# Optimization experiments

Measured on AMD Instinct MI355X. Metric: run time of the kernel, lower is better.

The kernel has to match this reference:

```python
import jax, jax.numpy as jnp
import numpy as np
from jax import lax

# ---- Loihi neuron constants (params['neuron'], params['simulation']) ----
VTH_MANT = 80
THETA = VTH_MANT * (1 << 6)          # 5120, vThMant scaled by 2^6 weight resolution
I_DECAY = 1024                        # current decay (12-bit fixed point)
V_DECAY = 128                         # voltage decay (12-bit fixed point)
WGT_EXP = 0
WGT_SCALE = 1 << (6 + WGT_EXP)        # 64
TS = 1.0

def _loihi_srm_kernel():
    # integer Loihi simulation of the PSP impulse response (slayerLoihi._calculateLoihiPSP)
    u = 1 << (6 + WGT_EXP)
    v = u
    ker = [v]
    while ker[-1] > 0:
        u = (u * (4096 - I_DECAY)) >> 12
        v = ((v * (4096 - V_DECAY)) >> 12) + u
        ker.append(v)
    return np.asarray(ker, np.float32) / (1 << 6)

SRM_KERNEL = _loihi_srm_kernel()      # ~180 taps, ker[0] = 1

def psp(x):
    # causal FIR over time: y[t] = sum_k x[t-k] * ker[k];  x: [B, C, T]
    B, C, T = x.shape
    K = SRM_KERNEL.shape[0]
    w = jnp.asarray(SRM_KERNEL[::-1].copy()).reshape(1, 1, K).astype(x.dtype)
    y = lax.conv_general_dilated(x.reshape(B * C, 1, T), w, (1,), [(K - 1, 0)],
                                 dimension_numbers=('NCH', 'OIH', 'NCH'))
    return y.reshape(B, C, T)

def _decay(x, d):
    # sign-symmetric arithmetic-shift decay, exactly as the Loihi CUDA kernel
    s = jnp.where(x >= 0, 1, -1).astype(jnp.int32)
    return s * ((s * x * (4096 - d)) >> 12)

def spike_loihi(w):
    # quantized integrate-and-fire; w: [B, C, T] float weighted input
    x = jnp.trunc(w * (WGT_SCALE / TS)).astype(jnp.int32)   # C-style int() truncation
    xt = jnp.moveaxis(x, -1, 0)                             # [T, B, C]
    z = jnp.zeros(x.shape[:-1], jnp.int32)
    def step(carry, xi):
        u, v = carry
        un = _decay(u, I_DECAY) + xi
        vn = _decay(v, V_DECAY) + un
        sp = vn >= THETA
        vn = jnp.where(sp, 0, vn)                           # hard reset on spike
        return (un, vn), (sp, vn)
    _, (s, vrec) = lax.scan(step, (z, z), xt)
    spike = jnp.moveaxis(s, 0, -1).astype(w.dtype) / TS
    voltage = jnp.moveaxis(vrec, 0, -1).astype(w.dtype)
    return spike, voltage

def delay_shift(x):
    # delayShift(x, 1): one-tick axonal delay along time
    return jnp.concatenate([jnp.zeros_like(x[..., :1]), x[..., :-1]], axis=-1)

def setup_inputs():
    key = jax.random.key(0)
    k1, k2, k3 = jax.random.split(key, 3)
    B, CIN, HID, COUT, T = 32, 512, 1024, 256, 512
    spike_input = (jax.random.uniform(k1, (B, CIN, 1, 1, T)) < 0.05).astype(jnp.float32)
    W1 = jax.random.normal(k2, (HID, CIN), jnp.float32) * 0.2
    W2 = jax.random.normal(k3, (COUT, HID), jnp.float32) * 0.2
    return {"spike_input": spike_input, "W1": W1, "W2": W2}

def reference(spike_input, W1, W2):
    x = spike_input[:, :, 0, 0, :]                          # [B, Cin, T]
    s1, _ = spike_loihi(psp(jnp.einsum('oi,bit->bot', W1, x)))
    s1 = delay_shift(s1)
    s2, _ = spike_loihi(psp(jnp.einsum('oh,bht->bot', W2, s1)))
    s2 = delay_shift(s2)
    return s2[:, :, None, None, :]                          # [B, Cout, 1, 1, T]
```

## Files before the change

### kernel.cpp

```cpp
#include <hip/hip_runtime.h>


#pragma clang fp contract(off)

constexpr int kT     = 512;
constexpr int kCIN   = 512;
constexpr int kHID   = 1024;
constexpr int kCOUT  = 256;
constexpr int kB     = 32;
constexpr int kTHETA = 5120;
constexpr int kOT1   = 16;
constexpr int kOT2   = 8;
constexpr int kHBP1  = 20;
constexpr int kHBP2  = 12;
constexpr int kSBP   = 516;
constexpr int kCURP  = 520;

__device__ __forceinline__ float2 pkmul(const float2 a, const float b) {
    return make_float2(a.x * b, a.y * b);
}
__device__ __forceinline__ float2 pkadd(const float2 a, const float2 b) {
    return make_float2(a.x + b.x, a.y + b.y);
}

__device__ __forceinline__ int decay_i(int x, int mult) {
    unsigned ax = (x >= 0) ? (unsigned)x : (0u - (unsigned)x);
    unsigned p  = ax * (unsigned)mult;
    int sh = ((int)p) >> 12;
    return (x >= 0) ? sh : (int)(0u - (unsigned)sh);
}

__device__ __forceinline__ void build_ker_f(float* kerf) {
    int u = 64, v = 64;
    kerf[0] = 1.0f;
    int i = 1;
    while (v > 0 && i < 96) {
        u = (u * 3072) >> 12;
        v = ((v * 3968) >> 12) + u;
        kerf[i++] = (float)v * 0.015625f;
    }
}

__global__ __launch_bounds__(256) void k0_pack(const float* __restrict__ X,
                                               unsigned* __restrict__ XPW) {
    const int tid = blockIdx.x * 256 + threadIdx.x;
    const int b = tid >> 13, rem = tid & 8191, w = rem >> 9, t = rem & 511;
    const float* xp = X + ((size_t)(b * kCIN + w * 32)) * kT + t;
    unsigned m = 0;
#pragma unroll
    for (int k = 0; k < 32; ++k)
        m |= (xp[(size_t)k * kT] != 0.0f ? 1u : 0u) << k;
    XPW[tid] = m;
}

#define GW16(MW, BASE) { unsigned m_ = (MW); while (m_) { \
    const int bi_ = __ffs(m_) - 1; m_ &= m_ - 1; const int ii_ = (BASE) + bi_; \
    const float4 f0 = *reinterpret_cast<const float4*>(&w0[ii_ * 4]); \
    const float4 f1 = *reinterpret_cast<const float4*>(&w1[ii_ * 4]); \
    const float4 f2 = *reinterpret_cast<const float4*>(&w2[ii_ * 4]); \
    const float4 f3 = *reinterpret_cast<const float4*>(&w3[ii_ * 4]); \
    A0 = pkadd(A0, make_float2(f0.x, f0.y)); A1 = pkadd(A1, make_float2(f0.z, f0.w)); \
    A2 = pkadd(A2, make_float2(f1.x, f1.y)); A3 = pkadd(A3, make_float2(f1.z, f1.w)); \
    A4 = pkadd(A4, make_float2(f2.x, f2.y)); A5 = pkadd(A5, make_float2(f2.z, f2.w)); \
    A6 = pkadd(A6, make_float2(f3.x, f3.y)); A7 = pkadd(A7, make_float2(f3.z, f3.w)); } }

__global__ __launch_bounds__(512) void k1_fused(const unsigned* __restrict__ XPW,
                                                const float* __restrict__ W,
                                                unsigned char* __restrict__ SPT) {
    __shared__ __align__(16) unsigned char regn[40960];
    __shared__ unsigned char sbuf[kOT1 * kSBP];
    __shared__ float kerf[96];

    float* w0  = reinterpret_cast<float*>(regn);
    float* w1  = reinterpret_cast<float*>(regn + 8192);
    float* w2  = reinterpret_cast<float*>(regn + 16384);
    float* w3  = reinterpret_cast<float*>(regn + 24576);
    float* hbf = reinterpret_cast<float*>(regn);
    int*   cur = reinterpret_cast<int*>(regn);

    const int t     = threadIdx.x;
    const int b     = blockIdx.x >> 6;
    const int oblk  = blockIdx.x & 63;
    const int obase = oblk * kOT1;

    if (t == 0) build_ker_f(kerf);
    for (int idx = t; idx < kOT1 * kCIN; idx += 512) {
        const int j = idx >> 9, i = idx & 511;
        float* wq = reinterpret_cast<float*>(regn + (j >> 2) * 8192);
        wq[i * 4 + (j & 3)] = W[(size_t)(obase + j) * kCIN + i];
    }
    __syncthreads();

    const unsigned* xw = XPW + ((size_t)b * 16) * kT + t;
    float2 A0 = make_float2(0.f, 0.f), A1 = A0, A2 = A0, A3 = A0,
           A4 = A0, A5 = A0, A6 = A0, A7 = A0;
    {
        const unsigned m0=xw[0],    m1=xw[512],  m2=xw[1024], m3=xw[1536],
                       m4=xw[2048], m5=xw[2560], m6=xw[3072], m7=xw[3584],
                       m8=xw[4096], m9=xw[4608], mA=xw[5120], mB=xw[5632],
                       mC=xw[6144], mD=xw[6656], mE=xw[7168], mF=xw[7680];
        GW16(m0,0)   GW16(m1,32)  GW16(m2,64)  GW16(m3,96)
        GW16(m4,128) GW16(m5,160) GW16(m6,192) GW16(m7,224)
        GW16(m8,256) GW16(m9,288) GW16(mA,320) GW16(mB,352)
        GW16(mC,384) GW16(mD,416) GW16(mE,448) GW16(mF,480)
    }
    __syncthreads();

    {
        float* hr = hbf + (size_t)t * kHBP1;
        *reinterpret_cast<float4*>(hr + 0)  = make_float4(A0.x, A0.y, A1.x, A1.y);
        *reinterpret_cast<float4*>(hr + 4)  = make_float4(A2.x, A2.y, A3.x, A3.y);
        *reinterpret_cast<float4*>(hr + 8)  = make_float4(A4.x, A4.y, A5.x, A5.y);
        *reinterpret_cast<float4*>(hr + 12) = make_float4(A6.x, A6.y, A7.x, A7.y);
    }
    __syncthreads();

    float2 c0 = make_float2(0.f, 0.f), c1 = c0, c2 = c0, c3 = c0,
           c4 = c0, c5 = c0, c6 = c0, c7 = c0;
    {
        const int kmax = min(t + 1, 88);
        for (int tau = kmax - 1; tau >= 0; --tau) {
            const float kv = kerf[tau];
            const float* hr = hbf + (size_t)(t - tau) * kHBP1;
            const float4 q0 = *reinterpret_cast<const float4*>(hr + 0);
            const float4 q1 = *reinterpret_cast<const float4*>(hr + 4);
            const float4 q2 = *reinterpret_cast<const float4*>(hr + 8);
            const float4 q3 = *reinterpret_cast<const float4*>(hr + 12);
            c0 = pkadd(c0, pkmul(make_float2(q0.x, q0.y), kv));
            c1 = pkadd(c1, pkmul(make_float2(q0.z, q0.w), kv));
            c2 = pkadd(c2, pkmul(make_float2(q1.x, q1.y), kv));
            c3 = pkadd(c3, pkmul(make_float2(q1.z, q1.w), kv));
            c4 = pkadd(c4, pkmul(make_float2(q2.x, q2.y), kv));
            c5 = pkadd(c5, pkmul(make_float2(q2.z, q2.w), kv));
            c6 = pkadd(c6, pkmul(make_float2(q3.x, q3.y), kv));
            c7 = pkadd(c7, pkmul(make_float2(q3.z, q3.w), kv));
        }
    }
    __syncthreads();

    cur[ 0 * kCURP + t] = (int)(c0.x * 64.0f);
    cur[ 1 * kCURP + t] = (int)(c0.y * 64.0f);
    cur[ 2 * kCURP + t] = (int)(c1.x * 64.0f);
    cur[ 3 * kCURP + t] = (int)(c1.y * 64.0f);
    cur[ 4 * kCURP + t] = (int)(c2.x * 64.0f);
    cur[ 5 * kCURP + t] = (int)(c2.y * 64.0f);
    cur[ 6 * kCURP + t] = (int)(c3.x * 64.0f);
    cur[ 7 * kCURP + t] = (int)(c3.y * 64.0f);
    cur[ 8 * kCURP + t] = (int)(c4.x * 64.0f);
    cur[ 9 * kCURP + t] = (int)(c4.y * 64.0f);
    cur[10 * kCURP + t] = (int)(c5.x * 64.0f);
    cur[11 * kCURP + t] = (int)(c5.y * 64.0f);
    cur[12 * kCURP + t] = (int)(c6.x * 64.0f);
    cur[13 * kCURP + t] = (int)(c6.y * 64.0f);
    cur[14 * kCURP + t] = (int)(c7.x * 64.0f);
    cur[15 * kCURP + t] = (int)(c7.y * 64.0f);
    __syncthreads();

    if (t < kOT1) {
        const int* cr = cur + t * kCURP;
        int u = 0, v = 0;
        sbuf[t * kSBP + 0] = 0;
        for (int s = 0; s < kT; ++s) {
            const int un = (int)((unsigned)decay_i(u, 3072) + (unsigned)cr[s]);
            int vn = (int)((unsigned)decay_i(v, 3968) + (unsigned)un);
            const int sp_ = (vn >= kTHETA) ? 1 : 0;
            if (sp_) vn = 0;
            u = un; v = vn;
            if (s + 1 < kT) sbuf[t * kSBP + s + 1] = (unsigned char)sp_;
        }
    }
    __syncthreads();

#pragma unroll
    for (int h = 0; h < 2; ++h) {
        unsigned byte = 0;
#pragma unroll
        for (int j = 0; j < 8; ++j)
            byte |= (unsigned)sbuf[(h * 8 + j) * kSBP + t] << j;
        SPT[((size_t)b * 128 + oblk * 2 + h) * kT + t] = (unsigned char)byte;
    }
}

#define GW8(MW, BASE) { unsigned m_ = (MW); while (m_) { \
    const int bi_ = __ffs(m_) - 1; m_ &= m_ - 1; const int ii_ = (BASE) + bi_; \
    const float4 lo = *reinterpret_cast<const float4*>(&wlo[ii_ * 4]); \
    const float4 hi = *reinterpret_cast<const float4*>(&whi[ii_ * 4]); \
    A0 = pkadd(A0, make_float2(lo.x, lo.y)); A1 = pkadd(A1, make_float2(lo.z, lo.w)); \
    A2 = pkadd(A2, make_float2(hi.x, hi.y)); A3 = pkadd(A3, make_float2(hi.z, hi.w)); } }

__global__ __launch_bounds__(512) void k2_fused(const unsigned char* __restrict__ SPT,
                                                const float* __restrict__ W,
                                                float* __restrict__ O) {
    __shared__ __align__(16) unsigned char regn[32768];
    __shared__ unsigned char sbuf[kOT2 * kSBP];
    __shared__ float kerf[96];

    float* wlo = reinterpret_cast<float*>(regn);
    float* whi = reinterpret_cast<float*>(regn + 16384);
    float* hbf = reinterpret_cast<float*>(regn);
    int*   cur = reinterpret_cast<int*>(regn);

    const int t     = threadIdx.x;
    const int b     = blockIdx.x >> 5;
    const int obase = (blockIdx.x & 31) * kOT2;

    if (t == 0) build_ker_f(kerf);
    for (int idx = t; idx < kOT2 * kHID; idx += 512) {
        const int j = idx >> 10, i = idx & 1023;
        const float w = W[(size_t)(obase + j) * kHID + i];
        if (j < 4) wlo[i * 4 + j] = w; else whi[i * 4 + (j - 4)] = w;
    }
    __syncthreads();

    const unsigned char* sp = SPT + (size_t)b * (128 * kT) + t;
    float2 A0 = make_float2(0.f, 0.f), A1 = A0, A2 = A0, A3 = A0;
    for (int wd = 0; wd < 32; ++wd) {
        const unsigned b0 = sp[(size_t)(4 * wd + 0) * kT];
        const unsigned b1 = sp[(size_t)(4 * wd + 1) * kT];
        const unsigned b2 = sp[(size_t)(4 * wd + 2) * kT];
        const unsigned b3 = sp[(size_t)(4 * wd + 3) * kT];
        const unsigned m = b0 | (b1 << 8) | (b2 << 16) | (b3 << 24);
        GW8(m, wd * 32)
    }
    __syncthreads();

    {
        float* hr = hbf + (size_t)t * kHBP2;
        *reinterpret_cast<float4*>(hr + 0) = make_float4(A0.x, A0.y, A1.x, A1.y);
        *reinterpret_cast<float4*>(hr + 4) = make_float4(A2.x, A2.y, A3.x, A3.y);
    }
    __syncthreads();

    float2 c0 = make_float2(0.f, 0.f), c1 = c0, c2 = c0, c3 = c0;
    {
        const int kmax = min(t + 1, 88);
        for (int tau = kmax - 1; tau >= 0; --tau) {
            const float kv = kerf[tau];
            const float* hr = hbf + (size_t)(t - tau) * kHBP2;
            const float4 q0 = *reinterpret_cast<const float4*>(hr + 0);
            const float4 q1 = *reinterpret_cast<const float4*>(hr + 4);
            c0 = pkadd(c0, pkmul(make_float2(q0.x, q0.y), kv));
            c1 = pkadd(c1, pkmul(make_float2(q0.z, q0.w), kv));
            c2 = pkadd(c2, pkmul(make_float2(q1.x, q1.y), kv));
            c3 = pkadd(c3, pkmul(make_float2(q1.z, q1.w), kv));
        }
    }
    __syncthreads();

    cur[0 * kCURP + t] = (int)(c0.x * 64.0f);
    cur[1 * kCURP + t] = (int)(c0.y * 64.0f);
    cur[2 * kCURP + t] = (int)(c1.x * 64.0f);
    cur[3 * kCURP + t] = (int)(c1.y * 64.0f);
    cur[4 * kCURP + t] = (int)(c2.x * 64.0f);
    cur[5 * kCURP + t] = (int)(c2.y * 64.0f);
    cur[6 * kCURP + t] = (int)(c3.x * 64.0f);
    cur[7 * kCURP + t] = (int)(c3.y * 64.0f);
    __syncthreads();

    if (t < kOT2) {
        const int* cr = cur + t * kCURP;
        int u = 0, v = 0;
        sbuf[t * kSBP + 0] = 0;
        for (int s = 0; s < kT; ++s) {
            const int un = (int)((unsigned)decay_i(u, 3072) + (unsigned)cr[s]);
            int vn = (int)((unsigned)decay_i(v, 3968) + (unsigned)un);
            const int sp2 = (vn >= kTHETA) ? 1 : 0;
            if (sp2) vn = 0;
            u = un; v = vn;
            if (s + 1 < kT) sbuf[t * kSBP + s + 1] = (unsigned char)sp2;
        }
    }
    __syncthreads();

    for (int idx = t; idx < kOT2 * kT; idx += 512) {
        const int j = idx >> 9, tt = idx & 511;
        O[((size_t)(b * kCOUT + obase + j)) * kT + tt] = (float)sbuf[j * kSBP + tt];
    }
}

__global__ void k_mark(float* __restrict__ out0, float v) {
    if (threadIdx.x == 0 && blockIdx.x == 0) out0[0] = v;
}

extern "C" void kernel_launch(void* const* d_in, const int* in_sizes, int n_in,
                              void* d_out, int out_size, void* d_ws, size_t ws_size,
                              hipStream_t stream) {
    const float* X  = (const float*)d_in[0];
    const float* W1 = (const float*)d_in[1];
    const float* W2 = (const float*)d_in[2];
    float* OUT = (float*)d_out;

    const size_t xpw_bytes = (size_t)kB * 16 * kT * 4;
    const size_t spt_bytes = (size_t)kB * 128 * kT;
    const size_t need = xpw_bytes + spt_bytes;

    if (n_in != 3 || in_sizes[0] != kB * kCIN * kT || in_sizes[1] != kHID * kCIN ||
        in_sizes[2] != kCOUT * kHID || out_size != kB * kCOUT * kT) {
        hipLaunchKernelGGL(k_mark, dim3(1), dim3(64), 0, stream, OUT, 7000001.0f);
        return;
    }
    if (ws_size < need || d_ws == nullptr) {
        const float v = (float)(8000000u + (unsigned)((ws_size >> 10) % 900000));
        hipLaunchKernelGGL(k_mark, dim3(1), dim3(64), 0, stream, OUT, v);
        return;
    }

    unsigned*      xpw = (unsigned*)d_ws;
    unsigned char* spt = (unsigned char*)d_ws + xpw_bytes;

    hipLaunchKernelGGL(k0_pack, dim3(kB * 16 * kT / 256), dim3(256), 0, stream,
                       X, xpw);
    hipLaunchKernelGGL(k1_fused, dim3(kB * (kHID / kOT1)), dim3(512), 0, stream,
                       xpw, W1, spt);
    hipLaunchKernelGGL(k2_fused, dim3(kB * (kCOUT / kOT2)), dim3(512), 0, stream,
                       spt, W2, OUT);
}
```

Baseline: 454.9 us.

## Register-block PSP convolution over time pairs and pack layer-1 spikes as 32-bit words

The causal PSP FIR is restructured so each of 256 threads computes two adjacent timesteps, with hidden rows split into even/odd shared buffers. Each loaded row pair is reused for two outputs, which halves LDS traffic per output. The SRM kernel moves to compile-time constant memory, removing the per-block serial build. The layer-1 spike bitmask is stored as interleaved 16-bit halves, so layer 2 reads one 32-bit word per 32 channels instead of assembling four bytes, and occupancy hints are added to the launch bounds. The trade-off is that only half the threads do the convolution, and the summation order changes, so the float rounding of the accumulations may differ slightly.

Result: faster. 395.9 us (-13.0%).

```diff
diff --git a/kernel.cpp b/kernel.cpp
--- a/kernel.cpp
+++ b/kernel.cpp
@@ -11,10 +11,25 @@
 constexpr int kTHETA = 5120;
 constexpr int kOT1   = 16;
 constexpr int kOT2   = 8;
-constexpr int kHBP1  = 20;
-constexpr int kHBP2  = 12;
+constexpr int kHP1   = 20;
+constexpr int kHP2   = 12;
 constexpr int kSBP   = 516;
-constexpr int kCURP  = 520;
+constexpr int kCURP  = 521;
+
+struct Ker { float v[96]; int n; };
+constexpr Ker mk_ker() {
+    Ker K{}; int u = 64, v = 64; K.v[0] = 1.0f; int i = 1;
+    while (v > 0 && i < 96) {
+        u = (u * 3072) >> 12;
+        v = ((v * 3968) >> 12) + u;
+        K.v[i++] = (float)v / 64.0f;
+    }
+    K.n = i; return K;
+}
+constexpr Ker KER = mk_ker();
+static_assert(KER.n == 88, "SRM kernel length must be 88");
+static_assert(KER.v[87] == 0.0f, "tap 87 must be the exact zero tail tap");
+__device__ __constant__ Ker KERC = mk_ker();
 
 __device__ __forceinline__ float2 pkmul(const float2 a, const float b) {
     return make_float2(a.x * b, a.y * b);
@@ -28,17 +43,6 @@
     unsigned p  = ax * (unsigned)mult;
     int sh = ((int)p) >> 12;
     return (x >= 0) ? sh : (int)(0u - (unsigned)sh);
-}
-
-__device__ __forceinline__ void build_ker_f(float* kerf) {
-    int u = 64, v = 64;
-    kerf[0] = 1.0f;
-    int i = 1;
-    while (v > 0 && i < 96) {
-        u = (u * 3072) >> 12;
-        v = ((v * 3968) >> 12) + u;
-        kerf[i++] = (float)v * 0.015625f;
-    }
 }
 
 __global__ __launch_bounds__(256) void k0_pack(const float* __restrict__ X,
@@ -64,26 +68,35 @@
     A4 = pkadd(A4, make_float2(f2.x, f2.y)); A5 = pkadd(A5, make_float2(f2.z, f2.w)); \
     A6 = pkadd(A6, make_float2(f3.x, f3.y)); A7 = pkadd(A7, make_float2(f3.z, f3.w)); } }
 
-__global__ __launch_bounds__(512) void k1_fused(const unsigned* __restrict__ XPW,
-                                                const float* __restrict__ W,
-                                                unsigned char* __restrict__ SPT) {
+#define ACC16(E0,E1,E2,E3,E4,E5,E6,E7, Q0,Q1,Q2,Q3, KV) \
+    E0 = pkadd(E0, pkmul(make_float2(Q0.x, Q0.y), (KV))); \
+    E1 = pkadd(E1, pkmul(make_float2(Q0.z, Q0.w), (KV))); \
+    E2 = pkadd(E2, pkmul(make_float2(Q1.x, Q1.y), (KV))); \
+    E3 = pkadd(E3, pkmul(make_float2(Q1.z, Q1.w), (KV))); \
+    E4 = pkadd(E4, pkmul(make_float2(Q2.x, Q2.y), (KV))); \
+    E5 = pkadd(E5, pkmul(make_float2(Q2.z, Q2.w), (KV))); \
+    E6 = pkadd(E6, pkmul(make_float2(Q3.x, Q3.y), (KV))); \
+    E7 = pkadd(E7, pkmul(make_float2(Q3.z, Q3.w), (KV)));
+
+__global__ __launch_bounds__(512, 6) void k1_fused(const unsigned* __restrict__ XPW,
+                                                   const float* __restrict__ W,
+                                                   unsigned short* __restrict__ SPW) {
     __shared__ __align__(16) unsigned char regn[40960];
     __shared__ unsigned char sbuf[kOT1 * kSBP];
-    __shared__ float kerf[96];
-
-    float* w0  = reinterpret_cast<float*>(regn);
-    float* w1  = reinterpret_cast<float*>(regn + 8192);
-    float* w2  = reinterpret_cast<float*>(regn + 16384);
-    float* w3  = reinterpret_cast<float*>(regn + 24576);
-    float* hbf = reinterpret_cast<float*>(regn);
-    int*   cur = reinterpret_cast<int*>(regn);
+
+    float* w0    = reinterpret_cast<float*>(regn);
+    float* w1    = reinterpret_cast<float*>(regn + 8192);
+    float* w2    = reinterpret_cast<float*>(regn + 16384);
+    float* w3    = reinterpret_cast<float*>(regn + 24576);
+    float* heven = reinterpret_cast<float*>(regn);
+    float* hodd  = reinterpret_cast<float*>(regn + 20480);
+    int*   cur   = reinterpret_cast<int*>(regn);
 
     const int t     = threadIdx.x;
     const int b     = blockIdx.x >> 6;
     const int oblk  = blockIdx.x & 63;
     const int obase = oblk * kOT1;
 
-    if (t == 0) build_ker_f(kerf);
     for (int idx = t; idx < kOT1 * kCIN; idx += 512) {
         const int j = idx >> 9, i = idx & 511;
         float* wq = reinterpret_cast<float*>(regn + (j >> 2) * 8192);
@@ -107,7 +120,7 @@
     __syncthreads();
 
     {
-        float* hr = hbf + (size_t)t * kHBP1;
+        float* hr = ((t & 1) ? hodd : heven) + (size_t)(t >> 1) * kHP1;
         *reinterpret_cast<float4*>(hr + 0)  = make_float4(A0.x, A0.y, A1.x, A1.y);
         *reinterpret_cast<float4*>(hr + 4)  = make_float4(A2.x, A2.y, A3.x, A3.y);
         *reinterpret_cast<float4*>(hr + 8)  = make_float4(A4.x, A4.y, A5.x, A5.y);
@@ -115,45 +128,65 @@
     }
     __syncthreads();
 
-    float2 c0 = make_float2(0.f, 0.f), c1 = c0, c2 = c0, c3 = c0,
-           c4 = c0, c5 = c0, c6 = c0, c7 = c0;
-    {
-        const int kmax = min(t + 1, 88);
-        for (int tau = kmax - 1; tau >= 0; --tau) {
-            const float kv = kerf[tau];
-            const float* hr = hbf + (size_t)(t - tau) * kHBP1;
-            const float4 q0 = *reinterpret_cast<const float4*>(hr + 0);
-            const float4 q1 = *reinterpret_cast<const float4*>(hr + 4);
-            const float4 q2 = *reinterpret_cast<const float4*>(hr + 8);
-            const float4 q3 = *reinterpret_cast<const float4*>(hr + 12);
-            c0 = pkadd(c0, pkmul(make_float2(q0.x, q0.y), kv));
-            c1 = pkadd(c1, pkmul(make_float2(q0.z, q0.w), kv));
-            c2 = pkadd(c2, pkmul(make_float2(q1.x, q1.y), kv));
-            c3 = pkadd(c3, pkmul(make_float2(q1.z, q1.w), kv));
-            c4 = pkadd(c4, pkmul(make_float2(q2.x, q2.y), kv));
-            c5 = pkadd(c5, pkmul(make_float2(q2.z, q2.w), kv));
-            c6 = pkadd(c6, pkmul(make_float2(q3.x, q3.y), kv));
-            c7 = pkadd(c7, pkmul(make_float2(q3.z, q3.w), kv));
-        }
-    }
-    __syncthreads();
-
-    cur[ 0 * kCURP + t] = (int)(c0.x * 64.0f);
-    cur[ 1 * kCURP + t] = (int)(c0.y * 64.0f);
-    cur[ 2 * kCURP + t] = (int)(c1.x * 64.0f);
-    cur[ 3 * kCURP + t] = (int)(c1.y * 64.0f);
-    cur[ 4 * kCURP + t] = (int)(c2.x * 64.0f);
-    cur[ 5 * kCURP + t] = (int)(c2.y * 64.0f);
-    cur[ 6 * kCURP + t] = (int)(c3.x * 64.0f);
-    cur[ 7 * kCURP + t] = (int)(c3.y * 64.0f);
-    cur[ 8 * kCURP + t] = (int)(c4.x * 64.0f);
-    cur[ 9 * kCURP + t] = (int)(c4.y * 64.0f);
-    cur[10 * kCURP + t] = (int)(c5.x * 64.0f);
-    cur[11 * kCURP + t] = (int)(c5.y * 64.0f);
-    cur[12 * kCURP + t] = (int)(c6.x * 64.0f);
-    cur[13 * kCURP + t] = (int)(c6.y * 64.0f);
-    cur[14 * kCURP + t] = (int)(c7.x * 64.0f);
-    cur[15 * kCURP + t] = (int)(c7.y * 64.0f);
+    float2 E0, E1, E2, E3, E4, E5, E6, E7, O0, O1, O2, O3, O4, O5, O6, O7;
+    E0=E1=E2=E3=E4=E5=E6=E7=O0=O1=O2=O3=O4=O5=O6=O7 = make_float2(0.f, 0.f);
+    const int q = t;
+    if (t < 256) {
+        for (int j = 0; j < 43; ++j) {
+            const int m = q - 43 + j;
+            const float t87 = KERC.v[87 - 2 * j];
+            const float t86 = KERC.v[86 - 2 * j];
+            const float t85 = KERC.v[85 - 2 * j];
+            if (m >= 0) {
+                const float* he = heven + (size_t)m * kHP1;
+                const float* ho = hodd  + (size_t)m * kHP1;
+                const float4 a0 = *reinterpret_cast<const float4*>(he + 0);
+                const float4 a1 = *reinterpret_cast<const float4*>(he + 4);
+                const float4 a2 = *reinterpret_cast<const float4*>(he + 8);
+                const float4 a3 = *reinterpret_cast<const float4*>(he + 12);
+                const float4 b0 = *reinterpret_cast<const float4*>(ho + 0);
+                const float4 b1 = *reinterpret_cast<const float4*>(ho + 4);
+                const float4 b2 = *reinterpret_cast<const float4*>(ho + 8);
+                const float4 b3 = *reinterpret_cast<const float4*>(ho + 12);
+                ACC16(E0,E1,E2,E3,E4,E5,E6,E7, a0,a1,a2,a3, t86)
+                ACC16(E0,E1,E2,E3,E4,E5,E6,E7, b0,b1,b2,b3, t85)
+                ACC16(O0,O1,O2,O3,O4,O5,O6,O7, a0,a1,a2,a3, t87)
+                ACC16(O0,O1,O2,O3,O4,O5,O6,O7, b0,b1,b2,b3, t86)
+            }
+        }
+        {
+            const float* he = heven + (size_t)q * kHP1;
+            const float* ho = hodd  + (size_t)q * kHP1;
+            const float4 a0 = *reinterpret_cast<const float4*>(he + 0);
+            const float4 a1 = *reinterpret_cast<const float4*>(he + 4);
+            const float4 a2 = *reinterpret_cast<const float4*>(he + 8);
+            const float4 a3 = *reinterpret_cast<const float4*>(he + 12);
+            const float4 b0 = *reinterpret_cast<const float4*>(ho + 0);
+            const float4 b1 = *reinterpret_cast<const float4*>(ho + 4);
+            const float4 b2 = *reinterpret_cast<const float4*>(ho + 8);
+            const float4 b3 = *reinterpret_cast<const float4*>(ho + 12);
+            const float v1 = KERC.v[1];
+            ACC16(E0,E1,E2,E3,E4,E5,E6,E7, a0,a1,a2,a3, 1.0f)
+            ACC16(O0,O1,O2,O3,O4,O5,O6,O7, a0,a1,a2,a3, v1)
+            ACC16(O0,O1,O2,O3,O4,O5,O6,O7, b0,b1,b2,b3, 1.0f)
+        }
+    }
+    __syncthreads();
+
+    if (t < 256) {
+#define CST1(CH, EV, OV) \
+        cur[(CH) * kCURP + 2 * q]     = (int)((EV) * 64.0f); \
+        cur[(CH) * kCURP + 2 * q + 1] = (int)((OV) * 64.0f);
+        CST1( 0, E0.x, O0.x) CST1( 1, E0.y, O0.y)
+        CST1( 2, E1.x, O1.x) CST1( 3, E1.y, O1.y)
+        CST1( 4, E2.x, O2.x) CST1( 5, E2.y, O2.y)
+        CST1( 6, E3.x, O3.x) CST1( 7, E3.y, O3.y)
+        CST1( 8, E4.x, O4.x) CST1( 9, E4.y, O4.y)
+        CST1(10, E5.x, O5.x) CST1(11, E5.y, O5.y)
+        CST1(12, E6.x, O6.x) CST1(13, E6.y, O6.y)
+        CST1(14, E7.x, O7.x) CST1(15, E7.y, O7.y)
+#undef CST1
+    }
     __syncthreads();
 
     if (t < kOT1) {
@@ -171,13 +204,15 @@
     }
     __syncthreads();
 
+    {
+        unsigned lo = 0, hi = 0;
 #pragma unroll
-    for (int h = 0; h < 2; ++h) {
-        unsigned byte = 0;
-#pragma unroll
-        for (int j = 0; j < 8; ++j)
-            byte |= (unsigned)sbuf[(h * 8 + j) * kSBP + t] << j;
-        SPT[((size_t)b * 128 + oblk * 2 + h) * kT + t] = (unsigned char)byte;
+        for (int j = 0; j < 8; ++j) {
+            lo |= (unsigned)sbuf[j * kSBP + t] << j;
+            hi |= (unsigned)sbuf[(8 + j) * kSBP + t] << j;
+        }
+        SPW[((((size_t)b * 32 + (oblk >> 1)) * kT) + t) * 2 + (oblk & 1)] =
+            (unsigned short)(lo | (hi << 8));
     }
 }
 
@@ -188,23 +223,28 @@
     A0 = pkadd(A0, make_float2(lo.x, lo.y)); A1 = pkadd(A1, make_float2(lo.z, lo.w)); \
     A2 = pkadd(A2, make_float2(hi.x, hi.y)); A3 = pkadd(A3, make_float2(hi.z, hi.w)); } }
 
-__global__ __launch_bounds__(512) void k2_fused(const unsigned char* __restrict__ SPT,
-                                                const float* __restrict__ W,
-                                                float* __restrict__ O) {
+#define ACC8(E0,E1,E2,E3, Q0,Q1, KV) \
+    E0 = pkadd(E0, pkmul(make_float2(Q0.x, Q0.y), (KV))); \
+    E1 = pkadd(E1, pkmul(make_float2(Q0.z, Q0.w), (KV))); \
+    E2 = pkadd(E2, pkmul(make_float2(Q1.x, Q1.y), (KV))); \
+    E3 = pkadd(E3, pkmul(make_float2(Q1.z, Q1.w), (KV)));
+
+__global__ __launch_bounds__(512, 8) void k2_fused(const unsigned* __restrict__ SPW,
+                                                   const float* __restrict__ W,
+                                                   float* __restrict__ O) {
     __shared__ __align__(16) unsigned char regn[32768];
     __shared__ unsigned char sbuf[kOT2 * kSBP];
-    __shared__ float kerf[96];
-
-    float* wlo = reinterpret_cast<float*>(regn);
-    float* whi = reinterpret_cast<float*>(regn + 16384);
-    float* hbf = reinterpret_cast<float*>(regn);
-    int*   cur = reinterpret_cast<int*>(regn);
+
+    float* wlo   = reinterpret_cast<float*>(regn);
+    float* whi   = reinterpret_cast<float*>(regn + 16384);
+    float* heven = reinterpret_cast<float*>(regn);
+    float* hodd  = reinterpret_cast<float*>(regn + 12288);
+    int*   cur   = reinterpret_cast<int*>(regn);
 
     const int t     = threadIdx.x;
     const int b     = blockIdx.x >> 5;
     const int obase = (blockIdx.x & 31) * kOT2;
 
-    if (t == 0) build_ker_f(kerf);
     for (int idx = t; idx < kOT2 * kHID; idx += 512) {
         const int j = idx >> 10, i = idx & 1023;
         const float w = W[(size_t)(obase + j) * kHID + i];
@@ -212,49 +252,69 @@
     }
     __syncthreads();
 
-    const unsigned char* sp = SPT + (size_t)b * (128 * kT) + t;
+    const unsigned* sp = SPW + ((size_t)b * 32) * kT + t;
     float2 A0 = make_float2(0.f, 0.f), A1 = A0, A2 = A0, A3 = A0;
-    for (int wd = 0; wd < 32; ++wd) {
-        const unsigned b0 = sp[(size_t)(4 * wd + 0) * kT];
-        const unsigned b1 = sp[(size_t)(4 * wd + 1) * kT];
-        const unsigned b2 = sp[(size_t)(4 * wd + 2) * kT];
-        const unsigned b3 = sp[(size_t)(4 * wd + 3) * kT];
-        const unsigned m = b0 | (b1 << 8) | (b2 << 16) | (b3 << 24);
-        GW8(m, wd * 32)
+#pragma unroll 4
+    for (int g = 0; g < 32; ++g) {
+        const unsigned m = sp[(size_t)g * kT];
+        GW8(m, g * 32)
     }
     __syncthreads();
 
     {
-        float* hr = hbf + (size_t)t * kHBP2;
+        float* hr = ((t & 1) ? hodd : heven) + (size_t)(t >> 1) * kHP2;
         *reinterpret_cast<float4*>(hr + 0) = make_float4(A0.x, A0.y, A1.x, A1.y);
         *reinterpret_cast<float4*>(hr + 4) = make_float4(A2.x, A2.y, A3.x, A3.y);
     }
     __syncthreads();
 
-    float2 c0 = make_float2(0.f, 0.f), c1 = c0, c2 = c0, c3 = c0;
-    {
-        const int kmax = min(t + 1, 88);
-        for (int tau = kmax - 1; tau >= 0; --tau) {
-            const float kv = kerf[tau];
-            const float* hr = hbf + (size_t)(t - tau) * kHBP2;
-            const float4 q0 = *reinterpret_cast<const float4*>(hr + 0);
-            const float4 q1 = *reinterpret_cast<const float4*>(hr + 4);
-            c0 = pkadd(c0, pkmul(make_float2(q0.x, q0.y), kv));
-            c1 = pkadd(c1, pkmul(make_float2(q0.z, q0.w), kv));
-            c2 = pkadd(c2, pkmul(make_float2(q1.x, q1.y), kv));
-            c3 = pkadd(c3, pkmul(make_float2(q1.z, q1.w), kv));
-        }
-    }
-    __syncthreads();
-
-    cur[0 * kCURP + t] = (int)(c0.x * 64.0f);
-    cur[1 * kCURP + t] = (int)(c0.y * 64.0f);
-    cur[2 * kCURP + t] = (int)(c1.x * 64.0f);
-    cur[3 * kCURP + t] = (int)(c1.y * 64.0f);
-    cur[4 * kCURP + t] = (int)(c2.x * 64.0f);
-    cur[5 * kCURP + t] = (int)(c2.y * 64.0f);
-    cur[6 * kCURP + t] = (int)(c3.x * 64.0f);
-    cur[7 * kCURP + t] = (int)(c3.y * 64.0f);
+    float2 E0, E1, E2, E3, O0, O1, O2, O3;
+    E0=E1=E2=E3=O0=O1=O2=O3 = make_float2(0.f, 0.f);
+    const int q = t;
+    if (t < 256) {
+        for (int j = 0; j < 43; ++j) {
+            const int m = q - 43 + j;
+            const float t87 = KERC.v[87 - 2 * j];
+            const float t86 = KERC.v[86 - 2 * j];
+            const float t85 = KERC.v[85 - 2 * j];
+            if (m >= 0) {
+                const float* he = heven + (size_t)m * kHP2;
+                const float* ho = hodd  + (size_t)m * kHP2;
+                const float4 a0 = *reinterpret_cast<const float4*>(he + 0);
+                const float4 a1 = *reinterpret_cast<const float4*>(he + 4);
+                const float4 b0 = *reinterpret_cast<const float4*>(ho + 0);
+                const float4 b1 = *reinterpret_cast<const float4*>(ho + 4);
+                ACC8(E0,E1,E2,E3, a0,a1, t86)
+                ACC8(E0,E1,E2,E3, b0,b1, t85)
+                ACC8(O0,O1,O2,O3, a0,a1, t87)
+                ACC8(O0,O1,O2,O3, b0,b1, t86)
+            }
+        }
+        {
+            const float* he = heven + (size_t)q * kHP2;
+            const float* ho = hodd  + (size_t)q * kHP2;
+            const float4 a0 = *reinterpret_cast<const float4*>(he + 0);
+            const float4 a1 = *reinterpret_cast<const float4*>(he + 4);
+            const float4 b0 = *reinterpret_cast<const float4*>(ho + 0);
+            const float4 b1 = *reinterpret_cast<const float4*>(ho + 4);
+            const float v1 = KERC.v[1];
+            ACC8(E0,E1,E2,E3, a0,a1, 1.0f)
+            ACC8(O0,O1,O2,O3, a0,a1, v1)
+            ACC8(O0,O1,O2,O3, b0,b1, 1.0f)
+        }
+    }
+    __syncthreads();
+
+    if (t < 256) {
+#define CST2(CH, EV, OV) \
+        cur[(CH) * kCURP + 2 * q]     = (int)((EV) * 64.0f); \
+        cur[(CH) * kCURP + 2 * q + 1] = (int)((OV) * 64.0f);
+        CST2(0, E0.x, O0.x) CST2(1, E0.y, O0.y)
+        CST2(2, E1.x, O1.x) CST2(3, E1.y, O1.y)
+        CST2(4, E2.x, O2.x) CST2(5, E2.y, O2.y)
+        CST2(6, E3.x, O3.x) CST2(7, E3.y, O3.y)
+#undef CST2
+    }
     __syncthreads();
 
     if (t < kOT2) {
@@ -291,8 +351,8 @@
     float* OUT = (float*)d_out;
 
     const size_t xpw_bytes = (size_t)kB * 16 * kT * 4;
-    const size_t spt_bytes = (size_t)kB * 128 * kT;
-    const size_t need = xpw_bytes + spt_bytes;
+    const size_t spw_bytes = (size_t)kB * 32 * kT * 4;
+    const size_t need = xpw_bytes + spw_bytes;
 
     if (n_in != 3 || in_sizes[0] != kB * kCIN * kT || in_sizes[1] != kHID * kCIN ||
         in_sizes[2] != kCOUT * kHID || out_size != kB * kCOUT * kT) {
@@ -305,13 +365,13 @@
         return;
     }
 
-    unsigned*      xpw = (unsigned*)d_ws;
-    unsigned char* spt = (unsigned char*)d_ws + xpw_bytes;
+    unsigned*       xpw = (unsigned*)d_ws;
+    unsigned short* spw = (unsigned short*)((char*)d_ws + xpw_bytes);
 
     hipLaunchKernelGGL(k0_pack, dim3(kB * 16 * kT / 256), dim3(256), 0, stream,
                        X, xpw);
     hipLaunchKernelGGL(k1_fused, dim3(kB * (kHID / kOT1)), dim3(512), 0, stream,
-                       xpw, W1, spt);
+                       xpw, W1, spw);
     hipLaunchKernelGGL(k2_fused, dim3(kB * (kCOUT / kOT2)), dim3(512), 0, stream,
-                       spt, W2, OUT);
-}
+                       (const unsigned*)spw, W2, OUT);
+}
```
